# Performance work log

Measured on AMD Instinct MI355X. Metric: run time of the kernel, lower is better.

The kernel has to match this reference:

```python
import jax, jax.numpy as jnp
import numpy as np

B, N, DIM, HID = 128, 4096, 16, 128

def _linear_init(key, fan_in, fan_out):
    # torch nn.Linear default: U(-1/sqrt(fan_in), 1/sqrt(fan_in))
    kw, kb = jax.random.split(key)
    bound = 1.0 / np.sqrt(fan_in)
    W = jax.random.uniform(kw, (fan_in, fan_out), minval=-bound, maxval=bound, dtype=jnp.float32)
    b = jax.random.uniform(kb, (fan_out,), minval=-bound, maxval=bound, dtype=jnp.float32)
    return W, b

def setup_inputs() -> dict:
    key = jax.random.key(0)
    ks = jax.random.split(key, 8)
    x = jax.random.normal(ks[0], (B, N, DIM), dtype=jnp.float32)
    adj_col = (jax.random.uniform(ks[1], (N,), dtype=jnp.float32) > 0.5).astype(jnp.float32)
    W_n2e, b_n2e = _linear_init(ks[2], 2 * DIM, HID)
    W_e2e, b_e2e = _linear_init(ks[3], HID, HID)
    W_e2n, b_e2n = _linear_init(ks[4], HID, HID)
    W_n2n, b_n2n = _linear_init(ks[5], HID, HID)
    W_out, b_out = _linear_init(ks[6], DIM + HID, DIM)
    return {"x": x, "adj_col": adj_col,
            "W_n2e": W_n2e, "b_n2e": b_n2e,
            "W_e2e": W_e2e, "b_e2e": b_e2e,
            "W_e2n": W_e2n, "b_e2n": b_e2n,
            "W_n2n": W_n2n, "b_n2n": b_n2n,
            "W_out": W_out, "b_out": b_out,
            "i": 0}

def reference(x, adj_col, W_n2e, b_n2e, W_e2e, b_e2e, W_e2n, b_e2n, W_n2n, b_n2n, W_out, b_out, i):
    starter = x                                        # [B, N, dim]
    ender = x[:, i, :][:, None, :]                     # [B, 1, dim]
    ender = jnp.broadcast_to(ender, starter.shape)     # [B, N, dim]
    h = jnp.concatenate([starter, ender], axis=2)      # [B, N, 2*dim]
    h = jax.nn.relu(h @ W_n2e + b_n2e)                 # [B, N, hid]
    h = jax.nn.relu(h @ W_e2e + b_e2e)                 # [B, N, hid]
    h = h * adj_col[None, :, None]                     # adjacency mask
    h = jnp.sum(h, axis=1)                             # [B, hid]
    h = jax.nn.relu(h @ W_e2n + b_e2n)
    h = jax.nn.relu(h @ W_n2n + b_n2n)
    h = jnp.concatenate([starter[:, i, :], h], axis=-1)  # [B, dim+hid]
    return h @ W_out + b_out                           # [B, dim]
```

## Files before the change

### kernel.cpp

```cpp
#include <hip/hip_runtime.h>
#include <hip/hip_bf16.h>

#define B_    128
#define N_    4096
#define DIM_  16
#define HID_  128
#define NT_   8
#define ROWS_ (N_ / NT_)

typedef __bf16 bf16x2 __attribute__((ext_vector_type(2)));
typedef __bf16 bf16x8 __attribute__((ext_vector_type(8)));
typedef float floatx16 __attribute__((ext_vector_type(16)));
typedef unsigned int u32;
typedef unsigned int u32x4 __attribute__((ext_vector_type(4)));

__device__ inline bf16x8 load_cvt8(const float* __restrict__ p) {
  const float4 u = *(const float4*)p;
  const float4 v = *(const float4*)(p + 4);
  bf16x8 r;
  r[0] = (__bf16)u.x; r[1] = (__bf16)u.y; r[2] = (__bf16)u.z; r[3] = (__bf16)u.w;
  r[4] = (__bf16)v.x; r[5] = (__bf16)v.y; r[6] = (__bf16)v.z; r[7] = (__bf16)v.w;
  return r;
}

__device__ inline u32 pk2(float a, float b) {
  bf16x2 p; p[0] = (__bf16)a; p[1] = (__bf16)b;
  return __builtin_bit_cast(u32, p);
}

__global__ __launch_bounds__(256, 3) void edge_kernel(
    const float* __restrict__ x, const float* __restrict__ adj,
    const float* __restrict__ W1, const float* __restrict__ b1,
    const float* __restrict__ W2, const float* __restrict__ b2,
    const int* __restrict__ ip, float* __restrict__ part)
{
  __shared__ __align__(16) __bf16 sW2[HID_ * HID_];
  __shared__ int   sIdx[ROWS_ + 128];
  __shared__ float sAcc[HID_];
  __shared__ float sB1[HID_];
  __shared__ float sEnder[DIM_];
  __shared__ int   sCnt;

  const int t  = threadIdx.x;
  const int b  = blockIdx.y;
  const int n0 = blockIdx.x * ROWS_;
  const int ii = __ldg(ip);

  const int wave = t >> 6, lane = t & 63;
  const int half = lane >> 5, l31 = lane & 31;
  const int g  = wave >> 1;
  const int ch = wave & 1;

  if (t == 0) sCnt = 0;
  if (t < HID_) sAcc[t] = 0.f;
  if (t < DIM_) sEnder[t] = x[((size_t)b * N_ + ii) * DIM_ + t];
  __syncthreads();

  #pragma unroll
  for (int r = t; r < ROWS_; r += 256) {
    const bool act = adj[n0 + r] != 0.f;
    const unsigned long long m = __ballot(act);
    int base = 0;
    if (lane == 0) base = atomicAdd(&sCnt, __popcll(m));
    base = __shfl(base, 0);
    if (act) {
      const int pre = __builtin_amdgcn_mbcnt_hi((u32)(m >> 32),
                      __builtin_amdgcn_mbcnt_lo((u32)m, 0));
      sIdx[base + pre] = n0 + r;
    }
  }

  #pragma unroll
  for (int e = 0; e < 8; ++e) {
    const int G = t * 8 + e;
    const int c = G >> 4, gg = G & 15;
    bf16x8 v;
    #pragma unroll
    for (int j = 0; j < 8; ++j) v[j] = (__bf16)W2[((gg << 3) + j) * HID_ + c];
    *(bf16x8*)&sW2[(c << 7) + ((gg ^ (c & 15)) << 3)] = v;
  }

  bf16x8 w1f[4];
  #pragma unroll
  for (int ft = 0; ft < 4; ++ft) {
    bf16x8 v;
    #pragma unroll
    for (int j = 0; j < 8; ++j)
      v[j] = (__bf16)W1[(half * 8 + j) * HID_ + (ft * 32 + l31)];
    w1f[ft] = v;
  }

  if (t < HID_) {
    float s = b1[t];
    #pragma unroll
    for (int k = 0; k < DIM_; ++k) s += sEnder[k] * W1[(DIM_ + k) * HID_ + t];
    sB1[t] = s;
  }

  const float bv0 = b2[ch * 64 + l31], bv1 = b2[ch * 64 + 32 + l31];

  __syncthreads();
  const int cnt = sCnt;
  const int nch64 = (cnt + 63) >> 6;
  const int end = nch64 * 64;
  for (int p = cnt + t; p < end + 64; p += 256) sIdx[p] = n0;

  bf16x8 a2f[4], onef;
  #pragma unroll
  for (int j = 0; j < 8; ++j) onef[j] = (__bf16)0.f;
  if (half == 0) { onef[0] = (__bf16)1.f; onef[1] = (__bf16)1.f; }
  #pragma unroll
  for (int ft = 0; ft < 4; ++ft) {
    bf16x8 v;
    #pragma unroll
    for (int j = 0; j < 8; ++j) v[j] = (__bf16)0.f;
    if (half == 0) {
      const float s = sB1[ft * 32 + l31];
      const __bf16 hi = (__bf16)s;
      v[0] = hi;
      v[1] = (__bf16)(s - (float)hi);
    }
    a2f[ft] = v;
  }
  __syncthreads();

  float sum0 = 0.f, sum1 = 0.f;
  floatx16 zf;
  #pragma unroll
  for (int r = 0; r < 16; ++r) zf[r] = 0.f;

  int cb = g * 32;
  bf16x8 xf;
  {
    const int row = sIdx[cb + l31];
    xf = load_cvt8(&x[((size_t)b * N_ + row) * DIM_ + half * 8]);
  }

  for (; cb < end; cb += 64) {
    const int nrow = sIdx[cb + 64 + l31];

    bf16x8 af[8];
    #pragma unroll
    for (int ft = 0; ft < 4; ++ft) {
      floatx16 hc = __builtin_amdgcn_mfma_f32_32x32x16_bf16(w1f[ft], xf, zf, 0, 0, 0);
      hc = __builtin_amdgcn_mfma_f32_32x32x16_bf16(a2f[ft], onef, hc, 0, 0, 0);
      #pragma unroll
      for (int sg = 0; sg < 2; ++sg) {
        float e0 = fmaxf(hc[8*sg+0], 0.f), e1 = fmaxf(hc[8*sg+1], 0.f);
        float e2 = fmaxf(hc[8*sg+2], 0.f), e3 = fmaxf(hc[8*sg+3], 0.f);
        float e4 = fmaxf(hc[8*sg+4], 0.f), e5 = fmaxf(hc[8*sg+5], 0.f);
        float e6 = fmaxf(hc[8*sg+6], 0.f), e7 = fmaxf(hc[8*sg+7], 0.f);
        const u32 lo0 = pk2(e0, e1), lo1 = pk2(e2, e3);
        const u32 hi0 = pk2(e4, e5), hi1 = pk2(e6, e7);
        const u32 sA = half ? lo0 : hi0;
        const u32 sB = half ? lo1 : hi1;
        const u32 rA = (u32)__shfl_xor((int)sA, 32);
        const u32 rB = (u32)__shfl_xor((int)sB, 32);
        u32x4 d;
        d[0] = half ? rA : lo0;
        d[1] = half ? rB : lo1;
        d[2] = half ? hi0 : rA;
        d[3] = half ? hi1 : rB;
        af[ft * 2 + sg] = __builtin_bit_cast(bf16x8, d);
      }
    }

    const bf16x8 nxf = load_cvt8(&x[((size_t)b * N_ + nrow) * DIM_ + half * 8]);

    floatx16 c0 = zf, c1 = zf;
    #pragma unroll
    for (int s = 0; s < 8; ++s) {
      const int gp = ((s << 1) + half) ^ (l31 & 15);
      const __bf16* wp = &sW2[((ch * 64 + l31) << 7) + (gp << 3)];
      const bf16x8 wb0 = *(const bf16x8*)(wp);
      const bf16x8 wb1 = *(const bf16x8*)(wp + (32 << 7));
      c0 = __builtin_amdgcn_mfma_f32_32x32x16_bf16(af[s], wb0, c0, 0, 0, 0);
      c1 = __builtin_amdgcn_mfma_f32_32x32x16_bf16(af[s], wb1, c1, 0, 0, 0);
    }

    if (cb + 32 <= cnt) {
      #pragma unroll
      for (int r = 0; r < 16; ++r) {
        sum0 += fmaxf(c0[r] + bv0, 0.f);
        sum1 += fmaxf(c1[r] + bv1, 0.f);
      }
    } else {
      #pragma unroll
      for (int r = 0; r < 16; ++r) {
        const int q = cb + (r & 3) + ((r >> 2) << 3) + (half << 2);
        if (q < cnt) {
          sum0 += fmaxf(c0[r] + bv0, 0.f);
          sum1 += fmaxf(c1[r] + bv1, 0.f);
        }
      }
    }
    xf = nxf;
  }

  sum0 += __shfl_xor(sum0, 32);
  sum1 += __shfl_xor(sum1, 32);
  if (half == 0) {
    atomicAdd(&sAcc[ch * 64 + l31],      sum0);
    atomicAdd(&sAcc[ch * 64 + 32 + l31], sum1);
  }
  __syncthreads();
  if (t < HID_) part[((size_t)b * NT_ + blockIdx.x) * HID_ + t] = sAcc[t];
}

__global__ void tail_kernel(
    const float* __restrict__ x, const float* __restrict__ part,
    const float* __restrict__ W3, const float* __restrict__ b3,
    const float* __restrict__ W4, const float* __restrict__ b4,
    const float* __restrict__ W5, const float* __restrict__ b5,
    const int* __restrict__ ip, float* __restrict__ out)
{
  const int b = blockIdx.x, t = threadIdx.x;
  __shared__ float s0[HID_], s1[HID_], s2[HID_], se[DIM_];
  const int ii = __ldg(ip);
  if (t < DIM_) se[t] = x[((size_t)b * N_ + ii) * DIM_ + t];
  float a = 0.f;
  #pragma unroll
  for (int p = 0; p < NT_; ++p) a += part[((size_t)b * NT_ + p) * HID_ + t];
  s0[t] = a;
  __syncthreads();
  float v = b3[t];
  #pragma unroll 16
  for (int k = 0; k < HID_; ++k) v += s0[k] * W3[k * HID_ + t];
  s1[t] = fmaxf(v, 0.f);
  __syncthreads();
  float w = b4[t];
  #pragma unroll 16
  for (int k = 0; k < HID_; ++k) w += s1[k] * W4[k * HID_ + t];
  s2[t] = fmaxf(w, 0.f);
  __syncthreads();
  if (t < DIM_) {
    float o = b5[t];
    #pragma unroll
    for (int k = 0; k < DIM_; ++k) o += se[k] * W5[k * DIM_ + t];
    #pragma unroll 16
    for (int k = 0; k < HID_; ++k) o += s2[k] * W5[(DIM_ + k) * DIM_ + t];
    out[b * DIM_ + t] = o;
  }
}

extern "C" void kernel_launch(void* const* d_in, const int* in_sizes, int n_in,
                              void* d_out, int out_size, void* d_ws, size_t ws_size,
                              hipStream_t stream) {
  const float* x   = (const float*)d_in[0];
  const float* adj = (const float*)d_in[1];
  const float* W1  = (const float*)d_in[2];
  const float* b1  = (const float*)d_in[3];
  const float* W2  = (const float*)d_in[4];
  const float* b2  = (const float*)d_in[5];
  const float* W3  = (const float*)d_in[6];
  const float* b3  = (const float*)d_in[7];
  const float* W4  = (const float*)d_in[8];
  const float* b4  = (const float*)d_in[9];
  const float* W5  = (const float*)d_in[10];
  const float* b5  = (const float*)d_in[11];
  const int*   ip  = (const int*)d_in[12];
  float* out  = (float*)d_out;
  float* part = (float*)d_ws;

  edge_kernel<<<dim3(NT_, B_), 256, 0, stream>>>(x, adj, W1, b1, W2, b2, ip, part);
  tail_kernel<<<B_, HID_, 0, stream>>>(x, part, W3, b3, W4, b4, W5, b5, ip, out);
}
```

Baseline: 138.4 us.

## Hold W2 fragments in registers and halve node tiles per batch

The W2 MFMA operand fragments are loaded from shared memory once, before the loop, and kept in 16 registers, so the loop no longer issues repeated LDS reads. The node dimension is split into 4 tiles instead of 8, giving each block more rows to amortize setup. Occupancy is lowered to 2 blocks per SIMD to make room for the extra registers. W1 is now staged through shared memory for coalesced loads. The trade is fewer blocks (512) and lower occupancy for less LDS traffic.

New measurement: 123.8 us. 10.6% less time.

```diff
diff --git a/kernel.cpp b/kernel.cpp
--- a/kernel.cpp
+++ b/kernel.cpp
@@ -5,7 +5,7 @@
 #define N_    4096
 #define DIM_  16
 #define HID_  128
-#define NT_   8
+#define NT_   4
 #define ROWS_ (N_ / NT_)
 
 typedef __bf16 bf16x2 __attribute__((ext_vector_type(2)));
@@ -28,14 +28,15 @@
   return __builtin_bit_cast(u32, p);
 }
 
-__global__ __launch_bounds__(256, 3) void edge_kernel(
+__global__ __launch_bounds__(256, 2) void edge_kernel(
     const float* __restrict__ x, const float* __restrict__ adj,
     const float* __restrict__ W1, const float* __restrict__ b1,
     const float* __restrict__ W2, const float* __restrict__ b2,
     const int* __restrict__ ip, float* __restrict__ part)
 {
   __shared__ __align__(16) __bf16 sW2[HID_ * HID_];
-  __shared__ int   sIdx[ROWS_ + 128];
+  __shared__ __align__(16) float sW1s[DIM_][HID_];
+  __shared__ int   sIdx[ROWS_ + 192];
   __shared__ float sAcc[HID_];
   __shared__ float sB1[HID_];
   __shared__ float sEnder[DIM_];
@@ -48,7 +49,7 @@
 
   const int wave = t >> 6, lane = t & 63;
   const int half = lane >> 5, l31 = lane & 31;
-  const int g  = wave >> 1;
+  const int rg = wave >> 1;
   const int ch = wave & 1;
 
   if (t == 0) sCnt = 0;
@@ -71,6 +72,9 @@
   }
 
   #pragma unroll
+  for (int e = t; e < DIM_ * HID_; e += 256) sW1s[e >> 7][e & 127] = W1[e];
+
+  #pragma unroll
   for (int e = 0; e < 8; ++e) {
     const int G = t * 8 + e;
     const int c = G >> 4, gg = G & 15;
@@ -80,16 +84,6 @@
     *(bf16x8*)&sW2[(c << 7) + ((gg ^ (c & 15)) << 3)] = v;
   }
 
-  bf16x8 w1f[4];
-  #pragma unroll
-  for (int ft = 0; ft < 4; ++ft) {
-    bf16x8 v;
-    #pragma unroll
-    for (int j = 0; j < 8; ++j)
-      v[j] = (__bf16)W1[(half * 8 + j) * HID_ + (ft * 32 + l31)];
-    w1f[ft] = v;
-  }
-
   if (t < HID_) {
     float s = b1[t];
     #pragma unroll
@@ -103,7 +97,29 @@
   const int cnt = sCnt;
   const int nch64 = (cnt + 63) >> 6;
   const int end = nch64 * 64;
-  for (int p = cnt + t; p < end + 64; p += 256) sIdx[p] = n0;
+  for (int p = cnt + t; p < end + 128; p += 256) sIdx[p] = n0;
+
+  bf16x8 w1f[4];
+  #pragma unroll
+  for (int ft = 0; ft < 4; ++ft) {
+    bf16x8 v;
+    #pragma unroll
+    for (int j = 0; j < 8; ++j) v[j] = (__bf16)sW1s[half * 8 + j][ft * 32 + l31];
+    w1f[ft] = v;
+  }
+
+  bf16x8 w2r[16];
+  {
+    const int c0 = ch * 64 + l31;
+    const __bf16* base0 = &sW2[(c0 << 7)];
+    const __bf16* base1 = &sW2[((c0 + 32) << 7)];
+    #pragma unroll
+    for (int s = 0; s < 8; ++s) {
+      const int gp = ((s << 1) + half) ^ (c0 & 15);
+      w2r[s]     = *(const bf16x8*)(base0 + (gp << 3));
+      w2r[8 + s] = *(const bf16x8*)(base1 + (gp << 3));
+    }
+  }
 
   bf16x8 a2f[4], onef;
   #pragma unroll
@@ -129,7 +145,7 @@
   #pragma unroll
   for (int r = 0; r < 16; ++r) zf[r] = 0.f;
 
-  int cb = g * 32;
+  int cb = rg * 32;
   bf16x8 xf;
   {
     const int row = sIdx[cb + l31];
@@ -170,12 +186,8 @@
     floatx16 c0 = zf, c1 = zf;
     #pragma unroll
     for (int s = 0; s < 8; ++s) {
-      const int gp = ((s << 1) + half) ^ (l31 & 15);
-      const __bf16* wp = &sW2[((ch * 64 + l31) << 7) + (gp << 3)];
-      const bf16x8 wb0 = *(const bf16x8*)(wp);
-      const bf16x8 wb1 = *(const bf16x8*)(wp + (32 << 7));
-      c0 = __builtin_amdgcn_mfma_f32_32x32x16_bf16(af[s], wb0, c0, 0, 0, 0);
-      c1 = __builtin_amdgcn_mfma_f32_32x32x16_bf16(af[s], wb1, c1, 0, 0, 0);
+      c0 = __builtin_amdgcn_mfma_f32_32x32x16_bf16(af[s], w2r[s],     c0, 0, 0, 0);
+      c1 = __builtin_amdgcn_mfma_f32_32x32x16_bf16(af[s], w2r[8 + s], c1, 0, 0, 0);
     }
 
     if (cb + 32 <= cnt) {
```
